# Kernel tuning notes

Measured on AMD Instinct MI355X. Metric: run time of the kernel, lower is better.

Reference implementation:

```python
import jax, jax.numpy as jnp
import numpy as np

TOPK = 2  # n_activated
HID, INTER, E, SHARED_INTER = 2048, 1408, 14, 2816


def setup_inputs() -> dict:
    key = jax.random.key(0)
    ks = jax.random.split(key, 11)
    s = 0.02  # weight init scale
    return {
        "x": jax.random.normal(ks[0], (4, 512, HID), jnp.float32),
        "gate_w": jax.random.normal(ks[1], (E, HID), jnp.float32) * s,
        "cls_w": jax.random.normal(ks[2], (E, HID), jnp.float32) * s,
        "extra_scale": jax.random.normal(ks[3], (E,), jnp.float32) * 0.1,
        "extra_bias": jax.random.normal(ks[4], (E,), jnp.float32) * 0.01,
        "wg": jax.random.normal(ks[5], (E, INTER, HID), jnp.float32) * s,
        "wu": jax.random.normal(ks[6], (E, INTER, HID), jnp.float32) * s,
        "wd": jax.random.normal(ks[7], (E, HID, INTER), jnp.float32) * s,
        "sg": jax.random.normal(ks[8], (SHARED_INTER, HID), jnp.float32) * s,
        "su": jax.random.normal(ks[9], (SHARED_INTER, HID), jnp.float32) * s,
        "sd": jax.random.normal(ks[10], (HID, SHARED_INTER), jnp.float32) * s,
    }


def reference(x, gate_w, cls_w, extra_scale, extra_bias, wg, wu, wd, sg, su, sd):
    shape = x.shape
    d = shape[-1]
    xf = x.reshape(-1, d)                      # [T, d]
    T = xf.shape[0]
    n_exp = gate_w.shape[0]

    # Router: scores = softmax(|classifier(x) * silu(gate(x))|)
    logits = (xf @ cls_w.T) * jax.nn.silu(xf @ gate_w.T)        # [T, E]
    scores = jax.nn.softmax(jnp.abs(logits).astype(jnp.float32), axis=-1)
    biased = scores + extra_bias[None, :]
    _, idx = jax.lax.top_k(biased, TOPK)                         # [T, K]
    orig = 1.0 + scores * extra_scale[None, :]
    w = jnp.take_along_axis(orig, idx, axis=1).astype(x.dtype)   # [T, K]

    # Dense combine weights: zero for unrouted (token, expert) pairs.
    combine = jnp.zeros((T, n_exp), x.dtype).at[
        jnp.arange(T)[:, None], idx].add(w)                      # [T, E]

    # Routed experts (SwiGLU MLPs), computed densely then masked-combined.
    g = jax.nn.silu(jnp.einsum('td,efd->etf', xf, wg))           # [E, T, f]
    u = jnp.einsum('td,efd->etf', xf, wu)
    o = jnp.einsum('etf,edf->etd', g * u, wd)                    # [E, T, d]
    y = jnp.einsum('etd,te->td', o, combine)                     # [T, d]

    # Shared expert on all tokens.
    z = (jax.nn.silu(xf @ sg.T) * (xf @ su.T)) @ sd.T            # [T, d]

    return (y + z).reshape(shape)
```

## Files before the change

kernel.cpp:

```cpp
#include <hip/hip_runtime.h>

#define HID 2048
#define INTER 1408
#define NEXP 14
#define SINTER 2816
#define TTOK 2048
#define BM 384
#define BK 64

#define GLU_SH 264
#define GLU_RT 308
#define DWN_SH 192
#define DWN_RT 448

typedef short bf16x8 __attribute__((ext_vector_type(8)));
typedef float f32x4 __attribute__((ext_vector_type(4)));
typedef unsigned short u16x8 __attribute__((ext_vector_type(8)));

__device__ __forceinline__ unsigned short f2bf(float f) {
    __bf16 b = (__bf16)f;
    return __builtin_bit_cast(unsigned short, b);
}
__device__ __forceinline__ float bf2f(unsigned short u) {
    unsigned v = (unsigned)u << 16;
    return __builtin_bit_cast(float, v);
}
__device__ __forceinline__ unsigned swz(unsigned b) { return b ^ (((b >> 7) & 7u) << 4); }

__device__ __forceinline__ void gload16(const void* g, void* l) {
    __builtin_amdgcn_global_load_lds((__attribute__((address_space(1))) void*)g,
                                     (__attribute__((address_space(3))) void*)l, 16, 0, 0);
}
__device__ __forceinline__ void bsync() {
    __builtin_amdgcn_sched_barrier(0);
    __builtin_amdgcn_s_barrier();
    __builtin_amdgcn_sched_barrier(0);
}
#define WAIT_LGKM0 asm volatile("s_waitcnt lgkmcnt(0)" ::: "memory")

__global__ void k_zero(int* cnt) {
    if ((int)threadIdx.x < NEXP) cnt[threadIdx.x] = 0;
}

__global__ __launch_bounds__(256) void k_xcvt(const float* __restrict__ x,
                                              unsigned short* __restrict__ xb) {
    size_t i = ((size_t)blockIdx.x * 256 + threadIdx.x) * 8;
    float4 a = *(const float4*)(x + i);
    float4 b = *(const float4*)(x + i + 4);
    u16x8 v;
    v[0] = f2bf(a.x); v[1] = f2bf(a.y); v[2] = f2bf(a.z); v[3] = f2bf(a.w);
    v[4] = f2bf(b.x); v[5] = f2bf(b.y); v[6] = f2bf(b.z); v[7] = f2bf(b.w);
    *(u16x8*)(xb + i) = v;
}

__global__ __launch_bounds__(256) void k_router(
    const float* __restrict__ x,
    const float* __restrict__ gate_w, const float* __restrict__ cls_w,
    const float* __restrict__ escale, const float* __restrict__ ebias,
    int* __restrict__ cnt, int* __restrict__ etok, float* __restrict__ ew) {
    const int lane = threadIdx.x & 63;
    const int tok = blockIdx.x * 4 + (threadIdx.x >> 6);
    const float* xr = x + (size_t)tok * HID;
    float xv[32];
#pragma unroll
    for (int i = 0; i < 32; i++) xv[i] = xr[lane + 64 * i];

    float sc[NEXP];
    float mx = 0.f;
#pragma unroll
    for (int e = 0; e < NEXP; e++) {
        const float* cw = cls_w + (size_t)e * HID;
        const float* gw = gate_w + (size_t)e * HID;
        float pc = 0.f, pg = 0.f;
#pragma unroll
        for (int i = 0; i < 32; i++) {
            float v = xv[i];
            pc = fmaf(v, cw[lane + 64 * i], pc);
            pg = fmaf(v, gw[lane + 64 * i], pg);
        }
#pragma unroll
        for (int o = 32; o >= 1; o >>= 1) {
            pc += __shfl_xor(pc, o);
            pg += __shfl_xor(pg, o);
        }
        float lg = pc * (pg / (1.f + __expf(-pg)));
        sc[e] = fabsf(lg);
        mx = fmaxf(mx, sc[e]);
    }
    float s = 0.f;
#pragma unroll
    for (int e = 0; e < NEXP; e++) { sc[e] = __expf(sc[e] - mx); s += sc[e]; }
    float inv = 1.f / s;
    int i1 = -1, i2 = -1;
    float b1 = -1e30f, b2 = -1e30f, v1 = 0.f, v2 = 0.f;
#pragma unroll
    for (int e = 0; e < NEXP; e++) {
        float sv = sc[e] * inv;
        float b = sv + ebias[e];
        if (b > b1) { b2 = b1; i2 = i1; v2 = v1; b1 = b; i1 = e; v1 = sv; }
        else if (b > b2) { b2 = b; i2 = e; v2 = sv; }
    }
    if (lane == 0) {
        float w1 = 1.f + v1 * escale[i1];
        float w2 = 1.f + v2 * escale[i2];
        int p1 = atomicAdd(&cnt[i1], 1);
        etok[i1 * TTOK + p1] = tok * 2;     ew[i1 * TTOK + p1] = w1;
        int p2 = atomicAdd(&cnt[i2], 1);
        etok[i2 * TTOK + p2] = tok * 2 + 1; ew[i2 * TTOK + p2] = w2;
    }
}

__global__ void k_offsets(const int* __restrict__ cnt, int* __restrict__ offs) {
    if (threadIdx.x == 0) {
        int a = 0;
        for (int e = 0; e < NEXP; e++) { offs[e] = a; a += cnt[e]; }
    }
}

__global__ __launch_bounds__(1024) void k_glu6(
    const unsigned short* __restrict__ xb,
    const float* __restrict__ wg, const float* __restrict__ wu,
    const float* __restrict__ sg, const float* __restrict__ su,
    unsigned short* __restrict__ abuf, unsigned short* __restrict__ hbuf,
    const int* __restrict__ cnt, const int* __restrict__ offs,
    const int* __restrict__ etok) {
    __shared__ alignas(16) unsigned short sA[2][BM * BK];
    __shared__ alignas(16) unsigned short sBg[64 * BK];
    __shared__ alignas(16) unsigned short sBu[64 * BK];

    const int bx = blockIdx.x, t = threadIdx.x;
    const int lane = t & 63, w = t >> 6;
    const int wm = w >> 1, wn = w & 1;
    const int fr = lane & 15, fo = lane >> 4;

    const bool routed = bx >= GLU_SH;
    int n0, m_start, m_stop, obase, Ntot;
    const float *Bg, *Bu;
    unsigned short* outp;
    const int* etk = nullptr;
    if (routed) {
        int rx = bx - GLU_SH;
        int e = rx / 22; n0 = (rx % 22) * 64;
        int M = cnt[e];
        if (M <= 0) return;
        m_start = 0; m_stop = M; obase = offs[e]; Ntot = INTER;
        Bg = wg + ((size_t)e * INTER + n0) * HID;
        Bu = wu + ((size_t)e * INTER + n0) * HID;
        outp = abuf; etk = etok + e * TTOK;
    } else {
        n0 = (bx / 6) * 64;
        m_start = (bx % 6) * BM; m_stop = min(TTOK, m_start + BM);
        obase = 0; Ntot = SINTER;
        Bg = sg + (size_t)n0 * HID;
        Bu = su + (size_t)n0 * HID;
        outp = hbuf;
    }

    const int brow = t >> 4, bc4 = (t & 15) * 4;
    const float* srcG = Bg + (size_t)brow * HID + bc4;
    const float* srcU = Bu + (size_t)brow * HID + bc4;
    const unsigned wBo = swz((unsigned)(brow * 128 + bc4 * 2));

    unsigned aoff[3][2], boff[2][2];
#pragma unroll
    for (int mi = 0; mi < 3; mi++)
#pragma unroll
        for (int ks = 0; ks < 2; ks++)
            aoff[mi][ks] = swz((unsigned)((wm * 48 + mi * 16 + fr) * 128 + ks * 64 + fo * 16));
#pragma unroll
    for (int nj = 0; nj < 2; nj++)
#pragma unroll
        for (int ks = 0; ks < 2; ks++)
            boff[nj][ks] = swz((unsigned)((wn * 32 + nj * 16 + fr) * 128 + ks * 64 + fo * 16));

    const int arow_off = lane >> 3;
    const int achunk = (lane & 7) ^ arow_off;

    for (int m0 = m_start; m0 < m_stop; m0 += BM) {
        const int rv = min(m_stop - m0, BM);
        const unsigned short* srcA[3];
#pragma unroll
        for (int j = 0; j < 3; j++) {
            int r = (w * 3 + j) * 8 + arow_off;
            int rr = r < rv ? r : rv - 1;
            int tok = routed ? (etk[m0 + rr] >> 1) : (m0 + rr);
            srcA[j] = xb + (size_t)tok * HID + achunk * 8;
        }

        f32x4 ag[3][2], au[3][2];
#pragma unroll
        for (int mi = 0; mi < 3; mi++)
#pragma unroll
            for (int nj = 0; nj < 2; nj++) { ag[mi][nj] = {0.f,0.f,0.f,0.f}; au[mi][nj] = {0.f,0.f,0.f,0.f}; }

#pragma unroll
        for (int j = 0; j < 3; j++)
            gload16(srcA[j], (char*)sA + (w * 3 + j) * 1024);
        float4 gC = *(const float4*)(srcG);
        float4 uC = *(const float4*)(srcU);
        float4 gN, uN;

        for (int kk = 0; kk < HID / BK; ++kk) {
            const int cur = kk & 1;
            bsync();
            if (kk + 1 < HID / BK) {
                const int k0n = (kk + 1) * BK;
#pragma unroll
                for (int j = 0; j < 3; j++)
                    gload16(srcA[j] + k0n, (char*)sA + (cur ^ 1) * (BM * BK * 2) + (w * 3 + j) * 1024);
                gN = *(const float4*)(srcG + k0n);
                uN = *(const float4*)(srcU + k0n);
            }
            __builtin_amdgcn_sched_barrier(0);
            {
                ushort4 vg, vu;
                vg.x = f2bf(gC.x); vg.y = f2bf(gC.y); vg.z = f2bf(gC.z); vg.w = f2bf(gC.w);
                vu.x = f2bf(uC.x); vu.y = f2bf(uC.y); vu.z = f2bf(uC.z); vu.w = f2bf(uC.w);
                *(ushort4*)((char*)sBg + wBo) = vg;
                *(ushort4*)((char*)sBu + wBo) = vu;
            }
            WAIT_LGKM0;
            bsync();
            const char* sAc = (const char*)sA + cur * (BM * BK * 2);
#pragma unroll
            for (int ks = 0; ks < 2; ++ks) {
                bf16x8 af[3], gf[2], uf[2];
#pragma unroll
                for (int mi = 0; mi < 3; mi++) af[mi] = *(const bf16x8*)(sAc + aoff[mi][ks]);
#pragma unroll
                for (int nj = 0; nj < 2; nj++) {
                    gf[nj] = *(const bf16x8*)((const char*)sBg + boff[nj][ks]);
                    uf[nj] = *(const bf16x8*)((const char*)sBu + boff[nj][ks]);
                }
#pragma unroll
                for (int mi = 0; mi < 3; mi++)
#pragma unroll
                    for (int nj = 0; nj < 2; nj++) {
                        ag[mi][nj] = __builtin_amdgcn_mfma_f32_16x16x32_bf16(af[mi], gf[nj], ag[mi][nj], 0, 0, 0);
                        au[mi][nj] = __builtin_amdgcn_mfma_f32_16x16x32_bf16(af[mi], uf[nj], au[mi][nj], 0, 0, 0);
                    }
            }
            gC = gN; uC = uN;
        }

        char* sH = (char*)sA;
#pragma unroll
        for (int mi = 0; mi < 3; mi++)
#pragma unroll
            for (int jj = 0; jj < 4; jj++) {
                int r = wm * 48 + mi * 16 + fo * 4 + jj;
#pragma unroll
                for (int nj = 0; nj < 2; nj++) {
                    int c = wn * 32 + nj * 16 + fr;
                    float g = ag[mi][nj][jj];
                    float u = au[mi][nj][jj];
                    float h = (g / (1.f + __expf(-g))) * u;
                    *(unsigned short*)(sH + swz((unsigned)(r * 128 + c * 2))) = f2bf(h);
                }
            }
        WAIT_LGKM0;
        bsync();
#pragma unroll
        for (int q = 0; q < 3; q++) {
            int idx = q * 1024 + t;
            int r = idx >> 3, c = idx & 7;
            if (r < rv) {
                uint4 v = *(const uint4*)(sH + swz((unsigned)(r * 128 + c * 16)));
                *(uint4*)(outp + (size_t)(obase + m0 + r) * Ntot + n0 + c * 8) = v;
            }
        }
        bsync();
    }
}

__global__ __launch_bounds__(1024) void k_down6(
    const unsigned short* __restrict__ abuf, const unsigned short* __restrict__ hbuf,
    const float* __restrict__ wd, const float* __restrict__ sd,
    unsigned short* __restrict__ slots,
    const int* __restrict__ cnt, const int* __restrict__ offs,
    const int* __restrict__ etok, const float* __restrict__ ew) {
    __shared__ alignas(16) unsigned short sA[2][BM * BK];
    __shared__ alignas(16) unsigned short sB[64 * BK];

    const int bx = blockIdx.x, t = threadIdx.x;
    const int lane = t & 63, w = t >> 6;
    const int wm = w >> 1, wn = w & 1;
    const int fr = lane & 15, fo = lane >> 4;

    const bool routed = bx >= DWN_SH;
    int n0, m_start, m_stop, K, KT;
    const float* W;
    const unsigned short* Abuf;
    size_t arow0 = 0;
    const int* etk = nullptr; const float* ewe = nullptr;
    if (routed) {
        int rx = bx - DWN_SH;
        int e = rx / 32; n0 = (rx % 32) * 64;
        int M = cnt[e];
        if (M <= 0) return;
        m_start = 0; m_stop = M;
        K = INTER; KT = INTER / BK;
        W = wd + (size_t)e * HID * INTER + (size_t)n0 * INTER;
        Abuf = abuf; arow0 = offs[e];
        etk = etok + e * TTOK; ewe = ew + e * TTOK;
    } else {
        n0 = (bx / 6) * 64;
        m_start = (bx % 6) * BM; m_stop = min(TTOK, m_start + BM);
        K = SINTER; KT = SINTER / BK;
        W = sd + (size_t)n0 * SINTER;
        Abuf = hbuf;
    }

    const int brow = t >> 4, bc4 = (t & 15) * 4;
    const float* srcB = W + (size_t)brow * K + bc4;
    const unsigned wBo = swz((unsigned)(brow * 128 + bc4 * 2));

    unsigned aoff[3][2], boff[2][2];
#pragma unroll
    for (int mi = 0; mi < 3; mi++)
#pragma unroll
        for (int ks = 0; ks < 2; ks++)
            aoff[mi][ks] = swz((unsigned)((wm * 48 + mi * 16 + fr) * 128 + ks * 64 + fo * 16));
#pragma unroll
    for (int nj = 0; nj < 2; nj++)
#pragma unroll
        for (int ks = 0; ks < 2; ks++)
            boff[nj][ks] = swz((unsigned)((wn * 32 + nj * 16 + fr) * 128 + ks * 64 + fo * 16));

    const int arow_off = lane >> 3;
    const int achunk = (lane & 7) ^ arow_off;

    for (int m0 = m_start; m0 < m_stop; m0 += BM) {
        const int rv = min(m_stop - m0, BM);
        const unsigned short* srcA[3];
#pragma unroll
        for (int j = 0; j < 3; j++) {
            int r = (w * 3 + j) * 8 + arow_off;
            int rr = r < rv ? r : rv - 1;
            srcA[j] = Abuf + (arow0 + m0 + rr) * (size_t)K + achunk * 8;
        }

        f32x4 ac[3][2];
#pragma unroll
        for (int mi = 0; mi < 3; mi++)
#pragma unroll
            for (int nj = 0; nj < 2; nj++) ac[mi][nj] = {0.f, 0.f, 0.f, 0.f};

#pragma unroll
        for (int j = 0; j < 3; j++)
            gload16(srcA[j], (char*)sA + (w * 3 + j) * 1024);
        float4 bC = *(const float4*)(srcB);
        float4 bN;

        for (int kk = 0; kk < KT; ++kk) {
            const int cur = kk & 1;
            bsync();
            if (kk + 1 < KT) {
                const int k0n = (kk + 1) * BK;
#pragma unroll
                for (int j = 0; j < 3; j++)
                    gload16(srcA[j] + k0n, (char*)sA + (cur ^ 1) * (BM * BK * 2) + (w * 3 + j) * 1024);
                bN = *(const float4*)(srcB + k0n);
            }
            __builtin_amdgcn_sched_barrier(0);
            {
                ushort4 v;
                v.x = f2bf(bC.x); v.y = f2bf(bC.y); v.z = f2bf(bC.z); v.w = f2bf(bC.w);
                *(ushort4*)((char*)sB + wBo) = v;
            }
            WAIT_LGKM0;
            bsync();
            const char* sAc = (const char*)sA + cur * (BM * BK * 2);
#pragma unroll
            for (int ks = 0; ks < 2; ++ks) {
                bf16x8 af[3], bf[2];
#pragma unroll
                for (int mi = 0; mi < 3; mi++) af[mi] = *(const bf16x8*)(sAc + aoff[mi][ks]);
#pragma unroll
                for (int nj = 0; nj < 2; nj++) bf[nj] = *(const bf16x8*)((const char*)sB + boff[nj][ks]);
#pragma unroll
                for (int mi = 0; mi < 3; mi++)
#pragma unroll
                    for (int nj = 0; nj < 2; nj++)
                        ac[mi][nj] = __builtin_amdgcn_mfma_f32_16x16x32_bf16(af[mi], bf[nj], ac[mi][nj], 0, 0, 0);
            }
            bC = bN;
        }

        char* sH = (char*)sA;
#pragma unroll
        for (int mi = 0; mi < 3; mi++)
#pragma unroll
            for (int jj = 0; jj < 4; jj++) {
                int r = wm * 48 + mi * 16 + fo * 4 + jj;
                float wt = 1.f;
                if (routed) wt = (r < rv) ? ewe[m0 + r] : 0.f;
#pragma unroll
                for (int nj = 0; nj < 2; nj++) {
                    int c = wn * 32 + nj * 16 + fr;
                    *(unsigned short*)(sH + swz((unsigned)(r * 128 + c * 2))) =
                        f2bf(ac[mi][nj][jj] * wt);
                }
            }
        WAIT_LGKM0;
        bsync();
#pragma unroll
        for (int q = 0; q < 3; q++) {
            int idx = q * 1024 + t;
            int r = idx >> 3, c = idx & 7;
            if (r < rv) {
                uint4 v = *(const uint4*)(sH + swz((unsigned)(r * 128 + c * 16)));
                int tok, slice;
                if (routed) { int entry = etk[m0 + r]; tok = entry >> 1; slice = entry & 1; }
                else        { tok = m0 + r; slice = 2; }
                *(uint4*)(slots + ((size_t)slice * TTOK + tok) * HID + n0 + c * 8) = v;
            }
        }
        bsync();
    }
}

__global__ __launch_bounds__(256) void k_final(float* __restrict__ out,
                                               const unsigned short* __restrict__ slots) {
    size_t i = ((size_t)blockIdx.x * 256 + threadIdx.x) * 8;
    u16x8 s0 = *(const u16x8*)(slots + i);
    u16x8 s1 = *(const u16x8*)(slots + (size_t)TTOK * HID + i);
    u16x8 s2 = *(const u16x8*)(slots + (size_t)2 * TTOK * HID + i);
    float4 o0, o1;
    o0.x = bf2f(s0[0]) + bf2f(s1[0]) + bf2f(s2[0]);
    o0.y = bf2f(s0[1]) + bf2f(s1[1]) + bf2f(s2[1]);
    o0.z = bf2f(s0[2]) + bf2f(s1[2]) + bf2f(s2[2]);
    o0.w = bf2f(s0[3]) + bf2f(s1[3]) + bf2f(s2[3]);
    o1.x = bf2f(s0[4]) + bf2f(s1[4]) + bf2f(s2[4]);
    o1.y = bf2f(s0[5]) + bf2f(s1[5]) + bf2f(s2[5]);
    o1.z = bf2f(s0[6]) + bf2f(s1[6]) + bf2f(s2[6]);
    o1.w = bf2f(s0[7]) + bf2f(s1[7]) + bf2f(s2[7]);
    *(float4*)(out + i) = o0;
    *(float4*)(out + i + 4) = o1;
}

extern "C" void kernel_launch(void* const* d_in, const int* in_sizes, int n_in,
                              void* d_out, int out_size, void* d_ws, size_t ws_size,
                              hipStream_t stream) {
    const float* x = (const float*)d_in[0];
    const float* gate_w = (const float*)d_in[1];
    const float* cls_w = (const float*)d_in[2];
    const float* escale = (const float*)d_in[3];
    const float* ebias = (const float*)d_in[4];
    const float* wg = (const float*)d_in[5];
    const float* wu = (const float*)d_in[6];
    const float* wd = (const float*)d_in[7];
    const float* sg = (const float*)d_in[8];
    const float* su = (const float*)d_in[9];
    const float* sd = (const float*)d_in[10];
    float* out = (float*)d_out;

    char* ws = (char*)d_ws;
    size_t o = 0;
    auto alloc = [&](size_t bytes) {
        char* p = ws + o;
        o += (bytes + 255) & ~(size_t)255;
        return p;
    };
    unsigned short* xb    = (unsigned short*)alloc((size_t)TTOK * HID * 2);
    unsigned short* hbuf  = (unsigned short*)alloc((size_t)TTOK * SINTER * 2);
    unsigned short* abuf  = (unsigned short*)alloc((size_t)2 * TTOK * INTER * 2);
    unsigned short* slots = (unsigned short*)alloc((size_t)3 * TTOK * HID * 2);
    int* cnt              = (int*)alloc(256);
    int* offs             = (int*)alloc(256);
    int* etok             = (int*)alloc((size_t)NEXP * TTOK * 4);
    float* ew             = (float*)alloc((size_t)NEXP * TTOK * 4);

    k_zero<<<1, 64, 0, stream>>>(cnt);
    k_xcvt<<<2048, 256, 0, stream>>>(x, xb);
    k_router<<<512, 256, 0, stream>>>(x, gate_w, cls_w, escale, ebias, cnt, etok, ew);
    k_offsets<<<1, 64, 0, stream>>>(cnt, offs);
    k_glu6<<<GLU_SH + GLU_RT, 1024, 0, stream>>>(
        xb, wg, wu, sg, su, abuf, hbuf, cnt, offs, etok);
    k_down6<<<DWN_SH + DWN_RT, 1024, 0, stream>>>(
        abuf, hbuf, wd, sd, slots, cnt, offs, etok, ew);
    k_final<<<2048, 256, 0, stream>>>(out, slots);
}
```

Measured before the change: 650.1 us.

## Widen down-proj N tile to 128 and fuse bf16 cast into router

The down-projection kernel now computes 128 output columns per block instead of 64, halving the grid. Each block therefore reads the A activations once for twice the output width, and the epilogue writes its two 64-column halves in sequence through shared memory. The separate x-to-bf16 conversion kernel is removed, and the router writes the bf16 copy of x from values it already loads. Launch bounds with an occupancy hint are added to both GEMM kernels. The cost is more accumulator registers per wave, fewer blocks to spread across CUs, and an extra barrier round in the epilogue.

```diff
diff --git a/kernel.cpp b/kernel.cpp
--- a/kernel.cpp
+++ b/kernel.cpp
@@ -10,8 +10,8 @@
 
 #define GLU_SH 264
 #define GLU_RT 308
-#define DWN_SH 192
-#define DWN_RT 448
+#define DWN_SH 96
+#define DWN_RT 224
 
 typedef short bf16x8 __attribute__((ext_vector_type(8)));
 typedef float f32x4 __attribute__((ext_vector_type(4)));
@@ -42,28 +42,21 @@
     if ((int)threadIdx.x < NEXP) cnt[threadIdx.x] = 0;
 }
 
-__global__ __launch_bounds__(256) void k_xcvt(const float* __restrict__ x,
-                                              unsigned short* __restrict__ xb) {
-    size_t i = ((size_t)blockIdx.x * 256 + threadIdx.x) * 8;
-    float4 a = *(const float4*)(x + i);
-    float4 b = *(const float4*)(x + i + 4);
-    u16x8 v;
-    v[0] = f2bf(a.x); v[1] = f2bf(a.y); v[2] = f2bf(a.z); v[3] = f2bf(a.w);
-    v[4] = f2bf(b.x); v[5] = f2bf(b.y); v[6] = f2bf(b.z); v[7] = f2bf(b.w);
-    *(u16x8*)(xb + i) = v;
-}
-
 __global__ __launch_bounds__(256) void k_router(
     const float* __restrict__ x,
     const float* __restrict__ gate_w, const float* __restrict__ cls_w,
     const float* __restrict__ escale, const float* __restrict__ ebias,
-    int* __restrict__ cnt, int* __restrict__ etok, float* __restrict__ ew) {
+    int* __restrict__ cnt, int* __restrict__ etok, float* __restrict__ ew,
+    unsigned short* __restrict__ xb) {
     const int lane = threadIdx.x & 63;
     const int tok = blockIdx.x * 4 + (threadIdx.x >> 6);
     const float* xr = x + (size_t)tok * HID;
     float xv[32];
 #pragma unroll
     for (int i = 0; i < 32; i++) xv[i] = xr[lane + 64 * i];
+    unsigned short* xbr = xb + (size_t)tok * HID;
+#pragma unroll
+    for (int i = 0; i < 32; i++) xbr[lane + 64 * i] = f2bf(xv[i]);
 
     float sc[NEXP];
     float mx = 0.f;
@@ -117,7 +110,7 @@
     }
 }
 
-__global__ __launch_bounds__(1024) void k_glu6(
+__global__ __launch_bounds__(1024, 4) void k_glu9(
     const unsigned short* __restrict__ xb,
     const float* __restrict__ wg, const float* __restrict__ wu,
     const float* __restrict__ sg, const float* __restrict__ su,
@@ -273,14 +266,14 @@
     }
 }
 
-__global__ __launch_bounds__(1024) void k_down6(
+__global__ __launch_bounds__(1024, 4) void k_down9(
     const unsigned short* __restrict__ abuf, const unsigned short* __restrict__ hbuf,
     const float* __restrict__ wd, const float* __restrict__ sd,
     unsigned short* __restrict__ slots,
     const int* __restrict__ cnt, const int* __restrict__ offs,
     const int* __restrict__ etok, const float* __restrict__ ew) {
     __shared__ alignas(16) unsigned short sA[2][BM * BK];
-    __shared__ alignas(16) unsigned short sB[64 * BK];
+    __shared__ alignas(16) unsigned short sB[128 * BK];
 
     const int bx = blockIdx.x, t = threadIdx.x;
     const int lane = t & 63, w = t >> 6;
@@ -295,7 +288,7 @@
     const int* etk = nullptr; const float* ewe = nullptr;
     if (routed) {
         int rx = bx - DWN_SH;
-        int e = rx / 32; n0 = (rx % 32) * 64;
+        int e = rx / 16; n0 = (rx % 16) * 128;
         int M = cnt[e];
         if (M <= 0) return;
         m_start = 0; m_stop = M;
@@ -304,28 +297,28 @@
         Abuf = abuf; arow0 = offs[e];
         etk = etok + e * TTOK; ewe = ew + e * TTOK;
     } else {
-        n0 = (bx / 6) * 64;
+        n0 = (bx / 6) * 128;
         m_start = (bx % 6) * BM; m_stop = min(TTOK, m_start + BM);
         K = SINTER; KT = SINTER / BK;
         W = sd + (size_t)n0 * SINTER;
         Abuf = hbuf;
     }
 
-    const int brow = t >> 4, bc4 = (t & 15) * 4;
-    const float* srcB = W + (size_t)brow * K + bc4;
-    const unsigned wBo = swz((unsigned)(brow * 128 + bc4 * 2));
-
-    unsigned aoff[3][2], boff[2][2];
+    const int brow = t >> 3, bc8 = (t & 7) * 8;
+    const float* srcB = W + (size_t)brow * K + bc8;
+    const unsigned wBo = swz((unsigned)(brow * 128 + bc8 * 2));
+
+    unsigned aoff[3][2], boff[4][2];
 #pragma unroll
     for (int mi = 0; mi < 3; mi++)
 #pragma unroll
         for (int ks = 0; ks < 2; ks++)
             aoff[mi][ks] = swz((unsigned)((wm * 48 + mi * 16 + fr) * 128 + ks * 64 + fo * 16));
 #pragma unroll
-    for (int nj = 0; nj < 2; nj++)
+    for (int nj = 0; nj < 4; nj++)
 #pragma unroll
         for (int ks = 0; ks < 2; ks++)
-            boff[nj][ks] = swz((unsigned)((wn * 32 + nj * 16 + fr) * 128 + ks * 64 + fo * 16));
+            boff[nj][ks] = swz((unsigned)((wn * 64 + nj * 16 + fr) * 128 + ks * 64 + fo * 16));
 
     const int arow_off = lane >> 3;
     const int achunk = (lane & 7) ^ arow_off;
@@ -340,17 +333,17 @@
             srcA[j] = Abuf + (arow0 + m0 + rr) * (size_t)K + achunk * 8;
         }
 
-        f32x4 ac[3][2];
+        f32x4 ac[3][4];
 #pragma unroll
         for (int mi = 0; mi < 3; mi++)
 #pragma unroll
-            for (int nj = 0; nj < 2; nj++) ac[mi][nj] = {0.f, 0.f, 0.f, 0.f};
+            for (int nj = 0; nj < 4; nj++) ac[mi][nj] = {0.f, 0.f, 0.f, 0.f};
 
 #pragma unroll
         for (int j = 0; j < 3; j++)
             gload16(srcA[j], (char*)sA + (w * 3 + j) * 1024);
-        float4 bC = *(const float4*)(srcB);
-        float4 bN;
+        float4 bC0 = *(const float4*)(srcB), bC1 = *(const float4*)(srcB + 4);
+        float4 bN0, bN1;
 
         for (int kk = 0; kk < KT; ++kk) {
             const int cur = kk & 1;
@@ -360,63 +353,70 @@
 #pragma unroll
                 for (int j = 0; j < 3; j++)
                     gload16(srcA[j] + k0n, (char*)sA + (cur ^ 1) * (BM * BK * 2) + (w * 3 + j) * 1024);
-                bN = *(const float4*)(srcB + k0n);
+                bN0 = *(const float4*)(srcB + k0n);
+                bN1 = *(const float4*)(srcB + k0n + 4);
             }
             __builtin_amdgcn_sched_barrier(0);
             {
-                ushort4 v;
-                v.x = f2bf(bC.x); v.y = f2bf(bC.y); v.z = f2bf(bC.z); v.w = f2bf(bC.w);
-                *(ushort4*)((char*)sB + wBo) = v;
+                bf16x8 v;
+                v[0]=(short)f2bf(bC0.x); v[1]=(short)f2bf(bC0.y); v[2]=(short)f2bf(bC0.z); v[3]=(short)f2bf(bC0.w);
+                v[4]=(short)f2bf(bC1.x); v[5]=(short)f2bf(bC1.y); v[6]=(short)f2bf(bC1.z); v[7]=(short)f2bf(bC1.w);
+                *(bf16x8*)((char*)sB + wBo) = v;
             }
             WAIT_LGKM0;
             bsync();
             const char* sAc = (const char*)sA + cur * (BM * BK * 2);
 #pragma unroll
             for (int ks = 0; ks < 2; ++ks) {
-                bf16x8 af[3], bf[2];
+                bf16x8 af[3], bf[4];
 #pragma unroll
                 for (int mi = 0; mi < 3; mi++) af[mi] = *(const bf16x8*)(sAc + aoff[mi][ks]);
 #pragma unroll
-                for (int nj = 0; nj < 2; nj++) bf[nj] = *(const bf16x8*)((const char*)sB + boff[nj][ks]);
+                for (int nj = 0; nj < 4; nj++) bf[nj] = *(const bf16x8*)((const char*)sB + boff[nj][ks]);
 #pragma unroll
                 for (int mi = 0; mi < 3; mi++)
 #pragma unroll
-                    for (int nj = 0; nj < 2; nj++)
+                    for (int nj = 0; nj < 4; nj++)
                         ac[mi][nj] = __builtin_amdgcn_mfma_f32_16x16x32_bf16(af[mi], bf[nj], ac[mi][nj], 0, 0, 0);
             }
-            bC = bN;
+            bC0 = bN0; bC1 = bN1;
         }
 
         char* sH = (char*)sA;
 #pragma unroll
-        for (int mi = 0; mi < 3; mi++)
-#pragma unroll
-            for (int jj = 0; jj < 4; jj++) {
-                int r = wm * 48 + mi * 16 + fo * 4 + jj;
-                float wt = 1.f;
-                if (routed) wt = (r < rv) ? ewe[m0 + r] : 0.f;
-#pragma unroll
-                for (int nj = 0; nj < 2; nj++) {
-                    int c = wn * 32 + nj * 16 + fr;
-                    *(unsigned short*)(sH + swz((unsigned)(r * 128 + c * 2))) =
-                        f2bf(ac[mi][nj][jj] * wt);
+        for (int p = 0; p < 2; p++) {
+            if (wn == p) {
+#pragma unroll
+                for (int mi = 0; mi < 3; mi++)
+#pragma unroll
+                    for (int jj = 0; jj < 4; jj++) {
+                        int r = wm * 48 + mi * 16 + fo * 4 + jj;
+                        float wt = 1.f;
+                        if (routed) wt = (r < rv) ? ewe[m0 + r] : 0.f;
+#pragma unroll
+                        for (int nj = 0; nj < 4; nj++) {
+                            int c = nj * 16 + fr;
+                            *(unsigned short*)(sH + swz((unsigned)(r * 128 + c * 2))) =
+                                f2bf(ac[mi][nj][jj] * wt);
+                        }
+                    }
+            }
+            WAIT_LGKM0;
+            bsync();
+#pragma unroll
+            for (int q = 0; q < 3; q++) {
+                int idx = q * 1024 + t;
+                int r = idx >> 3, c = idx & 7;
+                if (r < rv) {
+                    uint4 v = *(const uint4*)(sH + swz((unsigned)(r * 128 + c * 16)));
+                    int tok, slice;
+                    if (routed) { int entry = etk[m0 + r]; tok = entry >> 1; slice = entry & 1; }
+                    else        { tok = m0 + r; slice = 2; }
+                    *(uint4*)(slots + ((size_t)slice * TTOK + tok) * HID + n0 + p * 64 + c * 8) = v;
                 }
             }
-        WAIT_LGKM0;
-        bsync();
-#pragma unroll
-        for (int q = 0; q < 3; q++) {
-            int idx = q * 1024 + t;
-            int r = idx >> 3, c = idx & 7;
-            if (r < rv) {
-                uint4 v = *(const uint4*)(sH + swz((unsigned)(r * 128 + c * 16)));
-                int tok, slice;
-                if (routed) { int entry = etk[m0 + r]; tok = entry >> 1; slice = entry & 1; }
-                else        { tok = m0 + r; slice = 2; }
-                *(uint4*)(slots + ((size_t)slice * TTOK + tok) * HID + n0 + c * 8) = v;
-            }
-        }
-        bsync();
+            bsync();
+        }
     }
 }
 
@@ -472,12 +472,11 @@
     float* ew             = (float*)alloc((size_t)NEXP * TTOK * 4);
 
     k_zero<<<1, 64, 0, stream>>>(cnt);
-    k_xcvt<<<2048, 256, 0, stream>>>(x, xb);
-    k_router<<<512, 256, 0, stream>>>(x, gate_w, cls_w, escale, ebias, cnt, etok, ew);
+    k_router<<<512, 256, 0, stream>>>(x, gate_w, cls_w, escale, ebias, cnt, etok, ew, xb);
     k_offsets<<<1, 64, 0, stream>>>(cnt, offs);
-    k_glu6<<<GLU_SH + GLU_RT, 1024, 0, stream>>>(
+    k_glu9<<<GLU_SH + GLU_RT, 1024, 0, stream>>>(
         xb, wg, wu, sg, su, abuf, hbuf, cnt, offs, etok);
-    k_down6<<<DWN_SH + DWN_RT, 1024, 0, stream>>>(
+    k_down9<<<DWN_SH + DWN_RT, 1024, 0, stream>>>(
         abuf, hbuf, wd, sd, slots, cnt, offs, etok, ew);
     k_final<<<2048, 256, 0, stream>>>(out, slots);
 }
```

Result: slower. 713.2 us (+9.7%).
